# Kernel tuning notes

Measured on AMD Instinct MI355X. Metric: run time of the kernel, lower is better.

## Reference

```python
import jax, jax.numpy as jnp
import numpy as np
from jax import lax

K = 3          # kernel size
K2 = K * K
STRIDE = 1
PAD = 1
DIL = 1


def _bilinear_sample(x_flat, py, px, H, W):
    """x_flat: [B, C, H*W]; py/px: [B, N] float sampling coords.
    Returns [B, C, N]; zero outside the image (matches DCNv2 CUDA kernel)."""
    y0 = jnp.floor(py)
    x0 = jnp.floor(px)
    dy = py - y0
    dx = px - x0
    y0i = y0.astype(jnp.int32)
    x0i = x0.astype(jnp.int32)

    def gather(yi, xi):
        valid = (yi >= 0) & (yi < H) & (xi >= 0) & (xi < W)
        idx = jnp.clip(yi, 0, H - 1) * W + jnp.clip(xi, 0, W - 1)  # [B, N]
        v = jnp.take_along_axis(x_flat, idx[:, None, :], axis=2)   # [B, C, N]
        return v * valid[:, None, :].astype(x_flat.dtype)

    w00 = ((1 - dy) * (1 - dx))[:, None, :]
    w01 = ((1 - dy) * dx)[:, None, :]
    w10 = (dy * (1 - dx))[:, None, :]
    w11 = (dy * dx)[:, None, :]
    out = gather(y0i, x0i) * w00
    out = out + gather(y0i, x0i + 1) * w01
    out = out + gather(y0i + 1, x0i) * w10
    out = out + gather(y0i + 1, x0i + 1) * w11
    return out


def setup_inputs() -> dict:
    key = jax.random.key(0)
    k1, k2, k3, k4, k5 = jax.random.split(key, 5)
    B, Cin, H, W = 4, 256, 64, 64
    Co = 256
    x = jax.random.normal(k1, (B, Cin, H, W), dtype=jnp.float32)
    # NOTE: original code zero-inits the offset/mask conv; we use small random
    # weights so the bilinear-sampling path is actually exercised.
    w_om = jax.random.normal(k2, (3 * K2, Cin, K, K), dtype=jnp.float32) * 0.01
    b_om = jax.random.normal(k3, (3 * K2,), dtype=jnp.float32) * 0.01
    w_dcn = jax.random.normal(k4, (Co, Cin, K, K), dtype=jnp.float32) * (1.0 / np.sqrt(Cin * K2))
    b_dcn = jax.random.normal(k5, (Co,), dtype=jnp.float32) * 0.01
    return {"x": x, "w_om": w_om, "b_om": b_om, "w_dcn": w_dcn, "b_dcn": b_dcn}


def _forward(x, w_om, b_om, w_dcn, b_dcn):
    B, Cin, H, W = x.shape
    Co = w_dcn.shape[0]
    # offset/mask conv (standard 3x3, pad 1, stride 1)
    om = lax.conv_general_dilated(x, w_om, (STRIDE, STRIDE), [(PAD, PAD), (PAD, PAD)],
                                  rhs_dilation=(DIL, DIL)) + b_om[None, :, None, None]
    Ho, Wo = om.shape[2], om.shape[3]
    o1 = om[:, :K2]            # dy  [B, K2, Ho, Wo]
    o2 = om[:, K2:2 * K2]      # dx
    mask = jax.nn.sigmoid(om[:, 2 * K2:])  # [B, K2, Ho, Wo]

    # base sampling grid: kernel position k = kh*K + kw
    kh = jnp.arange(K2, dtype=jnp.float32) // K
    kw = jnp.arange(K2, dtype=jnp.float32) % K
    base_y = (jnp.arange(Ho, dtype=jnp.float32) * STRIDE - PAD)[None, :] + (kh * DIL)[:, None]  # [K2, Ho]
    base_x = (jnp.arange(Wo, dtype=jnp.float32) * STRIDE - PAD)[None, :] + (kw * DIL)[:, None]  # [K2, Wo]

    py = base_y[None, :, :, None] + o1  # [B, K2, Ho, Wo]
    px = base_x[None, :, None, :] + o2

    N = K2 * Ho * Wo
    x_flat = x.reshape(B, Cin, H * W)
    sampled = _bilinear_sample(x_flat, py.reshape(B, N), px.reshape(B, N), H, W)  # [B, Cin, N]
    sampled = sampled.reshape(B, Cin, K2, Ho * Wo)
    sampled = sampled * mask.reshape(B, 1, K2, Ho * Wo)

    w = w_dcn.reshape(Co, Cin, K2)
    out = jnp.einsum('bckn,ock->bon', sampled, w) + b_dcn[None, :, None]
    out = jax.nn.relu(out)  # only_dcn=False, bn=False -> ReLU
    return out.reshape(B, Co, Ho, Wo)


def reference(x, w_om, b_om, w_dcn, b_dcn):
    return _forward(x, w_om, b_om, w_dcn, b_dcn)
```

## Files before the change

### kernel.cpp

```cpp
#include <hip/hip_runtime.h>
#include <math.h>

typedef _Float16 f16x8 __attribute__((ext_vector_type(8)));
typedef float f32x4 __attribute__((ext_vector_type(4)));
typedef unsigned short ushort_t;

#define HW 4096
#define MFMA16 __builtin_amdgcn_mfma_f32_16x16x32_f16

__device__ __forceinline__ ushort_t f2h_u(float v) {
    union { _Float16 h; ushort_t u; } cv; cv.h = (_Float16)v; return cv.u;
}
__device__ __forceinline__ f16x8 splat8(float v) {
    _Float16 h = (_Float16)v;
    f16x8 r;
    #pragma unroll
    for (int i = 0; i < 8; ++i) r[i] = h;
    return r;
}
__device__ __forceinline__ void bar_lds() {
    asm volatile("s_waitcnt lgkmcnt(0)" ::: "memory");
    __builtin_amdgcn_s_barrier();
}

__global__ __launch_bounds__(256) void prep(
    const float* __restrict__ x, const float* __restrict__ w_dcn,
    const float* __restrict__ w_om,
    ushort_t* __restrict__ w16, ushort_t* __restrict__ wom16,
    ushort_t* __restrict__ xT)
{
    __shared__ ushort_t lds[64 * 256];
    int tid = threadIdx.x;
    if (blockIdx.x < 2592) {
        int flat = blockIdx.x * 256 + tid;
        if (flat < 589824) {
            int kk = flat & 31, co = (flat >> 5) & 255, c8 = (flat >> 13) & 7, k = flat >> 16;
            w16[flat] = f2h_u(w_dcn[(size_t)(co * 256 + c8 * 32 + kk) * 9 + k]);
        } else {
            int o = flat - 589824;
            int kk = o & 31, m = (o >> 5) & 31, c8 = (o >> 10) & 7, k = o >> 13;
            float v = (m < 27) ? w_om[(size_t)(m * 256 + c8 * 32 + kk) * 9 + k] : 0.0f;
            wom16[o] = f2h_u(v);
        }
        return;
    }
    int xb_id = blockIdx.x - 2592;
    int b    = xb_id >> 6;
    int pos0 = (xb_id & 63) * 64;
    int posw = tid & 63;
    int ciq  = tid >> 6;
    const float* xb = x + (size_t)b * 256 * HW + pos0 + posw;
    #pragma unroll
    for (int it = 0; it < 8; ++it) {
        int ci = it * 32 + ciq * 8;
        f16x8 hv;
        #pragma unroll
        for (int j = 0; j < 8; ++j)
            hv[j] = (_Float16)xb[(size_t)(ci + j) * HW];
        int off = posw * 512 + ((ci * 2) ^ ((posw & 7) << 4));
        *(f16x8*)((char*)lds + off) = hv;
    }
    __syncthreads();
    int posr = tid >> 2;
    int cg   = tid & 3;
    char* dst = (char*)(xT + ((size_t)(b * HW) + pos0 + posr) * 256);
    #pragma unroll
    for (int u = 0; u < 8; ++u) {
        int cB = u * 64 + cg * 16;
        f16x8 hv = *(const f16x8*)((const char*)lds + posr * 512 + (cB ^ ((posr & 7) << 4)));
        *(f16x8*)(dst + cB) = hv;
    }
}

__global__ __launch_bounds__(512) void om_fused(
    const ushort_t* __restrict__ xT, const ushort_t* __restrict__ wom16,
    const float* __restrict__ b_om,
    float* __restrict__ py, float* __restrict__ px, float* __restrict__ msk)
{
    int bid = blockIdx.x;
    int b  = bid >> 6;
    int ho = bid & 63;
    int tid = threadIdx.x;
    int s  = tid >> 6;
    int l  = tid & 63;
    int kb = l >> 4, c16 = l & 15;

    __shared__ float sOm[8][2048];

    f32x4 zv = {0.f, 0.f, 0.f, 0.f};
    f32x4 acc[2][4];
    #pragma unroll
    for (int i = 0; i < 2; ++i)
        #pragma unroll
        for (int j = 0; j < 4; ++j) acc[i][j] = zv;
    f16x8 hz;
    #pragma unroll
    for (int j = 0; j < 8; ++j) hz[j] = (_Float16)0.0f;

    const ushort_t* xTb = xT + (size_t)b * HW * 256;

    for (int k9 = 0; k9 < 9; ++k9) {
        int kh = k9 / 3, kw = k9 - kh * 3;
        int y = ho - 1 + kh;
        bool yv = (y >= 0) & (y < 64);
        int yc = min(max(y, 0), 63);
        const ushort_t* wp = wom16 + ((size_t)((k9 * 8 + s) * 32 + c16)) * 32 + kb * 8;
        f16x8 a0 = *(const f16x8*)wp;
        f16x8 a1 = *(const f16x8*)(wp + 512);
        f16x8 bf[4];
        #pragma unroll
        for (int jt = 0; jt < 4; ++jt) {
            int wox = jt * 16 + c16 + kw - 1;
            bool v = yv & (wox >= 0) & (wox < 64);
            int woc = min(max(wox, 0), 63);
            const ushort_t* sp = xTb + ((size_t)(yc * 64 + woc)) * 256 + s * 32 + kb * 8;
            f16x8 bv = *(const f16x8*)sp;
            bf[jt] = v ? bv : hz;
        }
        #pragma unroll
        for (int jt = 0; jt < 4; ++jt) {
            acc[0][jt] = MFMA16(a0, bf[jt], acc[0][jt], 0, 0, 0);
            acc[1][jt] = MFMA16(a1, bf[jt], acc[1][jt], 0, 0, 0);
        }
    }
    #pragma unroll
    for (int i = 0; i < 2; ++i)
        #pragma unroll
        for (int jt = 0; jt < 4; ++jt)
            #pragma unroll
            for (int r = 0; r < 4; ++r)
                sOm[s][(i * 16 + kb * 4 + r) * 64 + jt * 16 + c16] = acc[i][jt][r];
    __syncthreads();

    int e0 = tid * 4;
    int m  = e0 >> 6;
    int pl = e0 & 63;
    if (m < 27) {
        f32x4 v = zv;
        #pragma unroll
        for (int w8 = 0; w8 < 8; ++w8)
            v += *(const f32x4*)&sOm[w8][e0];
        float bias = b_om[m];
        int pos = ho * 64 + pl;
        if (m < 9) {
            int kh = m / 3;
            float* o = py + (size_t)(b * 9 + m) * HW + pos;
            #pragma unroll
            for (int j = 0; j < 4; ++j)
                o[j] = (float)(ho - 1 + kh) + v[j] + bias;
        } else if (m < 18) {
            int k = m - 9, kw = k % 3;
            float* o = px + (size_t)(b * 9 + k) * HW + pos;
            #pragma unroll
            for (int j = 0; j < 4; ++j)
                o[j] = (float)(pl + j - 1 + kw) + v[j] + bias;
        } else {
            int k = m - 18;
            float* o = msk + (size_t)(b * 9 + k) * HW + pos;
            #pragma unroll
            for (int j = 0; j < 4; ++j)
                o[j] = 1.0f / (1.0f + expf(-(v[j] + bias)));
        }
    }
}

__global__ __launch_bounds__(1024, 1) void dcn_fused(
    const ushort_t* __restrict__ xT, const ushort_t* __restrict__ w16,
    const float* __restrict__ b_dcn,
    const float* __restrict__ py, const float* __restrict__ px,
    const float* __restrict__ msk, float* __restrict__ out)
{
    int bid  = blockIdx.x;
    int b    = bid >> 6;
    int pos0 = (bid & 63) * 64;
    int tid  = threadIdx.x;
    int h    = tid >> 9;
    int t5   = tid & 511;
    int w    = t5 >> 6, l = t5 & 63;
    int kb   = l >> 4, c16 = l & 15;
    int g8   = t5 & 7, spos = t5 >> 3;
    int c0   = h * 18;

    __shared__ __align__(16) ushort_t sB2[2][2][4096];
    __shared__ float sR[512 * 33];

    ushort_t (&sB)[2][4096] = sB2[h];

    const ushort_t* xTb   = xT + (size_t)b * HW * 256;
    const ushort_t* wbase = w16 + (size_t)(w * 32 + c16) * 32 + kb * 8;

    f32x4 zv = {0.f, 0.f, 0.f, 0.f};
    f32x4 acc[2][4];
    #pragma unroll
    for (int i = 0; i < 2; ++i)
        #pragma unroll
        for (int j = 0; j < 4; ++j) acc[i][j] = zv;

    int o00 = 0, o01 = 0, o10 = 0, o11 = 0;
    float tw00 = 0.f, tw01 = 0.f, tw10 = 0.f, tw11 = 0.f;
    f32x4 wA, wB;
    f16x8 gA00, gA01, gA10, gA11;
    f16x8 gB00, gB01, gB10, gB11;
    f16x8 aA00, aA01, aA10, aA11;
    f16x8 aB00, aB01, aB10, aB11;

#define UPD(K9)                                                               \
    do {                                                                      \
        size_t gidx = (size_t)(b * 9 + (K9)) * HW + pos0 + spos;              \
        float fy = py[gidx], fx = px[gidx], mv = msk[gidx];                   \
        float y0f = floorf(fy), x0f = floorf(fx);                             \
        int y0 = (int)y0f, x0 = (int)x0f;                                     \
        float dy = fy - y0f, dx = fx - x0f;                                   \
        bool vy0 = (y0 >= 0) & (y0 < 64);                                     \
        bool vy1 = (y0 >= -1) & (y0 < 63);                                    \
        bool vx0 = (x0 >= 0) & (x0 < 64);                                     \
        bool vx1 = (x0 >= -1) & (x0 < 63);                                    \
        int y0c = min(max(y0, 0), 63), y1c = min(max(y0 + 1, 0), 63);         \
        int x0c = min(max(x0, 0), 63), x1c = min(max(x0 + 1, 0), 63);         \
        o00 = (y0c * 64 + x0c) * 256; o01 = (y0c * 64 + x1c) * 256;           \
        o10 = (y1c * 64 + x0c) * 256; o11 = (y1c * 64 + x1c) * 256;           \
        tw00 = (vy0 && vx0) ? (1.f - dy) * (1.f - dx) * mv : 0.f;             \
        tw01 = (vy0 && vx1) ? (1.f - dy) * dx * mv : 0.f;                     \
        tw10 = (vy1 && vx0) ? dy * (1.f - dx) * mv : 0.f;                     \
        tw11 = (vy1 && vx1) ? dy * dx * mv : 0.f;                             \
    } while (0)

#define ISS(S, CHUNK)                                                         \
    do {                                                                      \
        int cio = ((CHUNK) & 3) * 64 + g8 * 8;                                \
        g##S##00 = *(const f16x8*)(xTb + o00 + cio);                          \
        g##S##01 = *(const f16x8*)(xTb + o01 + cio);                          \
        g##S##10 = *(const f16x8*)(xTb + o10 + cio);                          \
        g##S##11 = *(const f16x8*)(xTb + o11 + cio);                          \
        w##S[0] = tw00; w##S[1] = tw01; w##S[2] = tw10; w##S[3] = tw11;       \
    } while (0)

#define CMB(S, CHUNK)                                                         \
    do {                                                                      \
        f16x8 s00 = splat8(w##S[0]), s01 = splat8(w##S[1]);                   \
        f16x8 s10 = splat8(w##S[2]), s11 = splat8(w##S[3]);                   \
        f16x8 res = g##S##00 * s00 + g##S##01 * s01                           \
                  + g##S##10 * s10 + g##S##11 * s11;                          \
        int byo = (g8 * 1024 + spos * 16) ^ (g8 << 4);                        \
        *(f16x8*)((char*)&sB[(CHUNK) & 1][0] + byo) = res;                    \
    } while (0)

#define LOADA(S, IT)                                                          \
    do {                                                                      \
        const ushort_t* ap = wbase + (size_t)(IT) * 16384;                    \
        a##S##00 = *(const f16x8*)ap;                                         \
        a##S##01 = *(const f16x8*)(ap + 512);                                 \
        a##S##10 = *(const f16x8*)(ap + 8192);                                \
        a##S##11 = *(const f16x8*)(ap + 8192 + 512);                          \
    } while (0)

#define MFMACORE(IT, S)                                                       \
    do {                                                                      \
        const char* bb = (const char*)&sB[(IT) & 1][0];                       \
        f16x8 b0[4], b1[4];                                                   \
        _Pragma("unroll")                                                     \
        for (int jt = 0; jt < 4; ++jt) {                                      \
            int p16 = (jt * 16 + c16) * 16;                                   \
            b0[jt] = *(const f16x8*)(bb + ((kb * 1024 + p16) ^ (kb << 4)));   \
            b1[jt] = *(const f16x8*)(bb + (((kb + 4) * 1024 + p16) ^ ((kb + 4) << 4))); \
        }                                                                     \
        _Pragma("unroll")                                                     \
        for (int jt = 0; jt < 4; ++jt) {                                      \
            acc[0][jt] = MFMA16(a##S##00, b0[jt], acc[0][jt], 0, 0, 0);       \
            acc[1][jt] = MFMA16(a##S##01, b0[jt], acc[1][jt], 0, 0, 0);       \
        }                                                                     \
        _Pragma("unroll")                                                     \
        for (int jt = 0; jt < 4; ++jt) {                                      \
            acc[0][jt] = MFMA16(a##S##10, b1[jt], acc[0][jt], 0, 0, 0);       \
            acc[1][jt] = MFMA16(a##S##11, b1[jt], acc[1][jt], 0, 0, 0);       \
        }                                                                     \
    } while (0)

    UPD(c0 >> 2);
    ISS(A, c0);
    ISS(B, c0 + 1);
    LOADA(A, c0);
    CMB(A, c0);
    bar_lds();

    for (int base = c0; base < c0 + 16; base += 2) {
        LOADA(B, base + 1);
        if (((base + 2) & 3) == 0) UPD((base + 2) >> 2);
        ISS(A, base + 2);
        CMB(B, base + 1);
        MFMACORE(base, A);
        bar_lds();
        LOADA(A, base + 2);
        ISS(B, base + 3);
        CMB(A, base + 2);
        MFMACORE(base + 1, B);
        bar_lds();
    }
    LOADA(B, c0 + 17);
    CMB(B, c0 + 17);
    MFMACORE(c0 + 16, A);
    bar_lds();
    MFMACORE(c0 + 17, B);

#undef UPD
#undef ISS
#undef CMB
#undef LOADA
#undef MFMACORE

    __syncthreads();
    if (h == 1) {
        #pragma unroll
        for (int i = 0; i < 2; ++i)
            #pragma unroll
            for (int jt = 0; jt < 4; ++jt)
                #pragma unroll
                for (int r = 0; r < 4; ++r)
                    sR[t5 * 33 + (i * 4 + jt) * 4 + r] = acc[i][jt][r];
    }
    __syncthreads();
    if (h == 0) {
        #pragma unroll
        for (int i = 0; i < 2; ++i)
            #pragma unroll
            for (int jt = 0; jt < 4; ++jt)
                #pragma unroll
                for (int r = 0; r < 4; ++r)
                    acc[i][jt][r] += sR[t5 * 33 + (i * 4 + jt) * 4 + r];
        #pragma unroll
        for (int i = 0; i < 2; ++i)
            #pragma unroll
            for (int r = 0; r < 4; ++r) {
                int co = w * 32 + i * 16 + kb * 4 + r;
                float bias = b_dcn[co];
                float* orow = out + (size_t)(b * 256 + co) * HW + pos0;
                #pragma unroll
                for (int jt = 0; jt < 4; ++jt)
                    orow[jt * 16 + c16] = fmaxf(acc[i][jt][r] + bias, 0.f);
            }
    }
}

extern "C" void kernel_launch(void* const* d_in, const int* in_sizes, int n_in,
                              void* d_out, int out_size, void* d_ws, size_t ws_size,
                              hipStream_t stream) {
    const float* x     = (const float*)d_in[0];
    const float* w_om  = (const float*)d_in[1];
    const float* b_om  = (const float*)d_in[2];
    const float* w_dcn = (const float*)d_in[3];
    const float* b_dcn = (const float*)d_in[4];
    float* out = (float*)d_out;

    float* ws = (float*)d_ws;
    float* py   = ws;
    float* px   = ws + 147456;
    float* msk  = ws + 294912;
    ushort_t* w16   = (ushort_t*)(ws + 442368);
    ushort_t* wom16 = (ushort_t*)(ws + 737280);
    ushort_t* xT    = (ushort_t*)(ws + 774144);

    prep     <<<2848, 256,  0, stream>>>(x, w_dcn, w_om, w16, wom16, xT);
    om_fused <<<256,  512,  0, stream>>>(xT, wom16, b_om, py, px, msk);
    dcn_fused<<<256,  1024, 0, stream>>>(xT, w16, b_dcn, py, px, msk, out);
}
```

Baseline: 59.94 us.

## Fuse offset/mask conv into DCN kernel and keep sampling params in LDS

Removes the separate om_fused launch. Each dcn_fused block now computes its own row's offset/mask conv with 16 waves splitting the taps, and writes py/px/mask into LDS instead of global memory. The block-to-tile mapping is remapped by XCD for locality. The prep weight-conversion blocks now do 4 elements per thread, and s_setprio is raised around the MFMA bursts. This saves one launch and a global round trip, at the cost of adding serial conv work at the start of each DCN block and larger LDS use.

```diff
diff --git a/kernel.cpp b/kernel.cpp
--- a/kernel.cpp
+++ b/kernel.cpp
@@ -31,20 +31,24 @@
 {
     __shared__ ushort_t lds[64 * 256];
     int tid = threadIdx.x;
-    if (blockIdx.x < 2592) {
-        int flat = blockIdx.x * 256 + tid;
-        if (flat < 589824) {
-            int kk = flat & 31, co = (flat >> 5) & 255, c8 = (flat >> 13) & 7, k = flat >> 16;
-            w16[flat] = f2h_u(w_dcn[(size_t)(co * 256 + c8 * 32 + kk) * 9 + k]);
-        } else {
-            int o = flat - 589824;
-            int kk = o & 31, m = (o >> 5) & 31, c8 = (o >> 10) & 7, k = o >> 13;
-            float v = (m < 27) ? w_om[(size_t)(m * 256 + c8 * 32 + kk) * 9 + k] : 0.0f;
-            wom16[o] = f2h_u(v);
+    if (blockIdx.x < 648) {
+        int base = (blockIdx.x * 256 + tid) * 4;
+        #pragma unroll
+        for (int j = 0; j < 4; ++j) {
+            int flat = base + j;
+            if (flat < 589824) {
+                int kk = flat & 31, co = (flat >> 5) & 255, c8 = (flat >> 13) & 7, k = flat >> 16;
+                w16[flat] = f2h_u(w_dcn[(size_t)(co * 256 + c8 * 32 + kk) * 9 + k]);
+            } else {
+                int o = flat - 589824;
+                int kk = o & 31, m = (o >> 5) & 31, c8 = (o >> 10) & 7, k = o >> 13;
+                float v = (m < 27) ? w_om[(size_t)(m * 256 + c8 * 32 + kk) * 9 + k] : 0.0f;
+                wom16[o] = f2h_u(v);
+            }
         }
         return;
     }
-    int xb_id = blockIdx.x - 2592;
+    int xb_id = blockIdx.x - 648;
     int b    = xb_id >> 6;
     int pos0 = (xb_id & 63) * 64;
     int posw = tid & 63;
@@ -72,124 +76,114 @@
     }
 }
 
-__global__ __launch_bounds__(512) void om_fused(
-    const ushort_t* __restrict__ xT, const ushort_t* __restrict__ wom16,
-    const float* __restrict__ b_om,
-    float* __restrict__ py, float* __restrict__ px, float* __restrict__ msk)
-{
-    int bid = blockIdx.x;
-    int b  = bid >> 6;
-    int ho = bid & 63;
-    int tid = threadIdx.x;
-    int s  = tid >> 6;
-    int l  = tid & 63;
-    int kb = l >> 4, c16 = l & 15;
-
-    __shared__ float sOm[8][2048];
-
-    f32x4 zv = {0.f, 0.f, 0.f, 0.f};
-    f32x4 acc[2][4];
-    #pragma unroll
-    for (int i = 0; i < 2; ++i)
-        #pragma unroll
-        for (int j = 0; j < 4; ++j) acc[i][j] = zv;
-    f16x8 hz;
-    #pragma unroll
-    for (int j = 0; j < 8; ++j) hz[j] = (_Float16)0.0f;
-
-    const ushort_t* xTb = xT + (size_t)b * HW * 256;
-
-    for (int k9 = 0; k9 < 9; ++k9) {
-        int kh = k9 / 3, kw = k9 - kh * 3;
-        int y = ho - 1 + kh;
-        bool yv = (y >= 0) & (y < 64);
-        int yc = min(max(y, 0), 63);
-        const ushort_t* wp = wom16 + ((size_t)((k9 * 8 + s) * 32 + c16)) * 32 + kb * 8;
-        f16x8 a0 = *(const f16x8*)wp;
-        f16x8 a1 = *(const f16x8*)(wp + 512);
-        f16x8 bf[4];
-        #pragma unroll
-        for (int jt = 0; jt < 4; ++jt) {
-            int wox = jt * 16 + c16 + kw - 1;
-            bool v = yv & (wox >= 0) & (wox < 64);
-            int woc = min(max(wox, 0), 63);
-            const ushort_t* sp = xTb + ((size_t)(yc * 64 + woc)) * 256 + s * 32 + kb * 8;
-            f16x8 bv = *(const f16x8*)sp;
-            bf[jt] = v ? bv : hz;
-        }
-        #pragma unroll
-        for (int jt = 0; jt < 4; ++jt) {
-            acc[0][jt] = MFMA16(a0, bf[jt], acc[0][jt], 0, 0, 0);
-            acc[1][jt] = MFMA16(a1, bf[jt], acc[1][jt], 0, 0, 0);
-        }
-    }
-    #pragma unroll
-    for (int i = 0; i < 2; ++i)
-        #pragma unroll
-        for (int jt = 0; jt < 4; ++jt)
-            #pragma unroll
-            for (int r = 0; r < 4; ++r)
-                sOm[s][(i * 16 + kb * 4 + r) * 64 + jt * 16 + c16] = acc[i][jt][r];
-    __syncthreads();
-
-    int e0 = tid * 4;
-    int m  = e0 >> 6;
-    int pl = e0 & 63;
-    if (m < 27) {
-        f32x4 v = zv;
-        #pragma unroll
-        for (int w8 = 0; w8 < 8; ++w8)
-            v += *(const f32x4*)&sOm[w8][e0];
-        float bias = b_om[m];
-        int pos = ho * 64 + pl;
-        if (m < 9) {
-            int kh = m / 3;
-            float* o = py + (size_t)(b * 9 + m) * HW + pos;
-            #pragma unroll
-            for (int j = 0; j < 4; ++j)
-                o[j] = (float)(ho - 1 + kh) + v[j] + bias;
-        } else if (m < 18) {
-            int k = m - 9, kw = k % 3;
-            float* o = px + (size_t)(b * 9 + k) * HW + pos;
-            #pragma unroll
-            for (int j = 0; j < 4; ++j)
-                o[j] = (float)(pl + j - 1 + kw) + v[j] + bias;
-        } else {
-            int k = m - 18;
-            float* o = msk + (size_t)(b * 9 + k) * HW + pos;
-            #pragma unroll
-            for (int j = 0; j < 4; ++j)
-                o[j] = 1.0f / (1.0f + expf(-(v[j] + bias)));
-        }
-    }
-}
-
 __global__ __launch_bounds__(1024, 1) void dcn_fused(
     const ushort_t* __restrict__ xT, const ushort_t* __restrict__ w16,
-    const float* __restrict__ b_dcn,
-    const float* __restrict__ py, const float* __restrict__ px,
-    const float* __restrict__ msk, float* __restrict__ out)
+    const ushort_t* __restrict__ wom16,
+    const float* __restrict__ b_om, const float* __restrict__ b_dcn,
+    float* __restrict__ out)
 {
-    int bid  = blockIdx.x;
-    int b    = bid >> 6;
-    int pos0 = (bid & 63) * 64;
+    int bid0 = blockIdx.x;
+    int xcd  = bid0 & 7, hi = bid0 >> 3;
+    int b    = xcd >> 1;
+    int pt   = hi | ((xcd & 1) << 5);
+    int ho   = pt;
+    int pos0 = pt * 64;
+
     int tid  = threadIdx.x;
     int h    = tid >> 9;
     int t5   = tid & 511;
-    int w    = t5 >> 6, l = t5 & 63;
-    int kb   = l >> 4, c16 = l & 15;
+    int w    = t5 >> 6, l5 = t5 & 63;
+    int kb   = l5 >> 4, c16 = l5 & 15;
     int g8   = t5 & 7, spos = t5 >> 3;
     int c0   = h * 18;
 
-    __shared__ __align__(16) ushort_t sB2[2][2][4096];
-    __shared__ float sR[512 * 33];
-
-    ushort_t (&sB)[2][4096] = sB2[h];
-
-    const ushort_t* xTb   = xT + (size_t)b * HW * 256;
+    __shared__ __align__(16) char smem[131072];
+    __shared__ float pyL[9][64], pxL[9][64], mskL[9][64];
+
+    float (*sOm)[2048] = (float (*)[2048])smem;
+    ushort_t (*sB)[4096] = (ushort_t (*)[4096])smem + h * 2;
+    float* sR = (float*)(smem + 32768);
+
+    const ushort_t* xTb = xT + (size_t)b * HW * 256;
+
+    f32x4 zv = {0.f, 0.f, 0.f, 0.f};
+
+    {
+        int s = tid >> 6;
+        int c = s & 7, p = s >> 3;
+        f32x4 acc[2][4];
+        #pragma unroll
+        for (int i = 0; i < 2; ++i)
+            #pragma unroll
+            for (int j = 0; j < 4; ++j) acc[i][j] = zv;
+        f16x8 hz;
+        #pragma unroll
+        for (int j = 0; j < 8; ++j) hz[j] = (_Float16)0.0f;
+
+        for (int tap = p; tap < 9; tap += 2) {
+            int kh = tap / 3, kw = tap - kh * 3;
+            int y = ho - 1 + kh;
+            bool yv = (y >= 0) & (y < 64);
+            int yc = min(max(y, 0), 63);
+            const ushort_t* wp = wom16 + ((size_t)((tap * 8 + c) * 32 + c16)) * 32 + kb * 8;
+            f16x8 a0 = *(const f16x8*)wp;
+            f16x8 a1 = *(const f16x8*)(wp + 512);
+            f16x8 bf[4];
+            #pragma unroll
+            for (int jt = 0; jt < 4; ++jt) {
+                int wox = jt * 16 + c16 + kw - 1;
+                bool v = yv & (wox >= 0) & (wox < 64);
+                int woc = min(max(wox, 0), 63);
+                const ushort_t* sp = xTb + ((size_t)(yc * 64 + woc)) * 256 + c * 32 + kb * 8;
+                f16x8 bv = *(const f16x8*)sp;
+                bf[jt] = v ? bv : hz;
+            }
+            #pragma unroll
+            for (int jt = 0; jt < 4; ++jt) {
+                acc[0][jt] = MFMA16(a0, bf[jt], acc[0][jt], 0, 0, 0);
+                acc[1][jt] = MFMA16(a1, bf[jt], acc[1][jt], 0, 0, 0);
+            }
+        }
+        #pragma unroll
+        for (int i = 0; i < 2; ++i)
+            #pragma unroll
+            for (int jt = 0; jt < 4; ++jt)
+                #pragma unroll
+                for (int r = 0; r < 4; ++r)
+                    sOm[s][(i * 16 + kb * 4 + r) * 64 + jt * 16 + c16] = acc[i][jt][r];
+        __syncthreads();
+
+        if (tid < 432) {
+            int e0 = tid * 4;
+            int m  = e0 >> 6;
+            int pl = e0 & 63;
+            f32x4 v = zv;
+            #pragma unroll
+            for (int s8 = 0; s8 < 16; ++s8)
+                v += *(const f32x4*)&sOm[s8][e0];
+            float bias = b_om[m];
+            if (m < 9) {
+                int kh = m / 3;
+                #pragma unroll
+                for (int j = 0; j < 4; ++j)
+                    pyL[m][pl + j] = (float)(ho - 1 + kh) + v[j] + bias;
+            } else if (m < 18) {
+                int k = m - 9, kw = k % 3;
+                #pragma unroll
+                for (int j = 0; j < 4; ++j)
+                    pxL[k][pl + j] = (float)(pl + j - 1 + kw) + v[j] + bias;
+            } else {
+                int k = m - 18;
+                #pragma unroll
+                for (int j = 0; j < 4; ++j)
+                    mskL[k][pl + j] = 1.0f / (1.0f + expf(-(v[j] + bias)));
+            }
+        }
+        __syncthreads();
+    }
+
     const ushort_t* wbase = w16 + (size_t)(w * 32 + c16) * 32 + kb * 8;
 
-    f32x4 zv = {0.f, 0.f, 0.f, 0.f};
     f32x4 acc[2][4];
     #pragma unroll
     for (int i = 0; i < 2; ++i)
@@ -206,8 +200,7 @@
 
 #define UPD(K9)                                                               \
     do {                                                                      \
-        size_t gidx = (size_t)(b * 9 + (K9)) * HW + pos0 + spos;              \
-        float fy = py[gidx], fx = px[gidx], mv = msk[gidx];                   \
+        float fy = pyL[(K9)][spos], fx = pxL[(K9)][spos], mv = mskL[(K9)][spos]; \
         float y0f = floorf(fy), x0f = floorf(fx);                             \
         int y0 = (int)y0f, x0 = (int)x0f;                                     \
         float dy = fy - y0f, dx = fx - x0f;                                   \
@@ -264,6 +257,7 @@
             b0[jt] = *(const f16x8*)(bb + ((kb * 1024 + p16) ^ (kb << 4)));   \
             b1[jt] = *(const f16x8*)(bb + (((kb + 4) * 1024 + p16) ^ ((kb + 4) << 4))); \
         }                                                                     \
+        __builtin_amdgcn_s_setprio(1);                                        \
         _Pragma("unroll")                                                     \
         for (int jt = 0; jt < 4; ++jt) {                                      \
             acc[0][jt] = MFMA16(a##S##00, b0[jt], acc[0][jt], 0, 0, 0);       \
@@ -274,6 +268,7 @@
             acc[0][jt] = MFMA16(a##S##10, b1[jt], acc[0][jt], 0, 0, 0);       \
             acc[1][jt] = MFMA16(a##S##11, b1[jt], acc[1][jt], 0, 0, 0);       \
         }                                                                     \
+        __builtin_amdgcn_s_setprio(0);                                        \
     } while (0)
 
     UPD(c0 >> 2);
@@ -351,15 +346,10 @@
     const float* b_dcn = (const float*)d_in[4];
     float* out = (float*)d_out;
 
-    float* ws = (float*)d_ws;
-    float* py   = ws;
-    float* px   = ws + 147456;
-    float* msk  = ws + 294912;
-    ushort_t* w16   = (ushort_t*)(ws + 442368);
-    ushort_t* wom16 = (ushort_t*)(ws + 737280);
-    ushort_t* xT    = (ushort_t*)(ws + 774144);
-
-    prep     <<<2848, 256,  0, stream>>>(x, w_dcn, w_om, w16, wom16, xT);
-    om_fused <<<256,  512,  0, stream>>>(xT, wom16, b_om, py, px, msk);
-    dcn_fused<<<256,  1024, 0, stream>>>(xT, w16, b_dcn, py, px, msk, out);
-}
+    ushort_t* w16   = (ushort_t*)d_ws;
+    ushort_t* wom16 = w16 + 589824;
+    ushort_t* xT    = wom16 + 73728;
+
+    prep     <<<904, 256,  0, stream>>>(x, w_dcn, w_om, w16, wom16, xT);
+    dcn_fused<<<256, 1024, 0, stream>>>(xT, w16, wom16, b_om, b_dcn, out);
+}
```

New measurement: 109.9 us. +83.4%, slower.
